# Optimization experiments

Measured on AMD Instinct MI355X. Metric: run time of the kernel, lower is better.

## Reference

```python
import jax, jax.numpy as jnp
import numpy as np

B, S, H = 2, 2048, 2048
NH, NKV, HD = 16, 8, 128
EPS = 1e-6
THETA = 10000.0
SCALE = HD ** -0.5


def setup_inputs() -> dict:
    key = jax.random.key(0)
    ks = jax.random.split(key, 6)
    return {
        "positions": jnp.tile(jnp.arange(S, dtype=jnp.int64 if jax.config.jax_enable_x64 else jnp.int32), (B, 1)),
        "hidden_states": jax.random.normal(ks[0], (B, S, H), jnp.float32),
        "residual": jax.random.normal(ks[1], (B, S, H), jnp.float32),
        "layernorm_weight": 1.0 + 0.02 * jax.random.normal(ks[2], (H,), jnp.float32),
        "qkv_weight": 0.02 * jax.random.normal(ks[3], ((NH + 2 * NKV) * HD, H), jnp.float32),
        "o_weight": 0.02 * jax.random.normal(ks[4], (H, NH * HD), jnp.float32),
        "q_norm_weight": 1.0 + 0.02 * jax.random.normal(ks[5], (HD,), jnp.float32),
        "k_norm_weight": jnp.ones((HD,), jnp.float32),
    }


def _rmsnorm(x, w, eps=EPS):
    return x * jax.lax.rsqrt(jnp.mean(x * x, axis=-1, keepdims=True) + eps) * w


def _rope(x, positions):
    # x: [B, S, h, HD]; neox-style rotate-half RoPE
    inv_freq = 1.0 / (THETA ** (jnp.arange(0, HD, 2, dtype=jnp.float32) / HD))
    ang = positions.astype(jnp.float32)[..., None] * inv_freq  # [B, S, HD/2]
    cos = jnp.cos(ang)[:, :, None, :]
    sin = jnp.sin(ang)[:, :, None, :]
    x1, x2 = jnp.split(x, 2, axis=-1)
    return jnp.concatenate([x1 * cos - x2 * sin, x2 * cos + x1 * sin], axis=-1)


def reference(positions, hidden_states, residual, layernorm_weight,
              qkv_weight, o_weight, q_norm_weight, k_norm_weight):
    # Fused RMSNorm + QKV projection (on unnormalized hidden_states)
    xn = _rmsnorm(hidden_states, layernorm_weight)
    qkv = jnp.einsum('bsh,oh->bso', xn, qkv_weight)  # [B, S, (NH+2*NKV)*HD]
    q, k, v = jnp.split(qkv, [NH * HD, (NH + NKV) * HD], axis=-1)
    q = q.reshape(B, S, NH, HD)
    k = k.reshape(B, S, NKV, HD)
    v = v.reshape(B, S, NKV, HD)
    # per-head q/k RMSNorm (q_norm in fused QKV kernel, k_norm inside attention)
    q = _rmsnorm(q, q_norm_weight)
    k = _rmsnorm(k, k_norm_weight)
    # RoPE
    q = _rope(q, positions)
    k = _rope(k, positions)
    # GQA: expand KV heads
    rep = NH // NKV
    k = jnp.repeat(k, rep, axis=2)
    v = jnp.repeat(v, rep, axis=2)
    # causal attention
    scores = jnp.einsum('bqhd,bkhd->bhqk', q, k) * SCALE
    causal = jnp.tril(jnp.ones((S, S), bool))
    scores = jnp.where(causal[None, None], scores, jnp.finfo(scores.dtype).min)
    probs = jax.nn.softmax(scores, axis=-1)
    attn = jnp.einsum('bhqk,bkhd->bqhd', probs, v).reshape(B, S, NH * HD)
    # fused output projection + residual add
    return jnp.einsum('bsd,hd->bsh', attn, o_weight) + residual
```

## Files before the change

kernel.cpp:

```cpp
#include <hip/hip_runtime.h>
#include <hip/hip_bf16.h>

typedef __attribute__((ext_vector_type(8))) short bf16x8;
typedef __attribute__((ext_vector_type(4))) float f32x4;

#define B_ 2
#define S_ 2048
#define H_ 2048
#define NH_ 16
#define NKV_ 8
#define HD_ 128
#define M_ (B_ * S_)
#define NQKV_ ((NH_ + 2 * NKV_) * HD_)
#define QK_SCALE 0.08838834764831845f

#define VMCNT(n) asm volatile("s_waitcnt vmcnt(" #n ")" ::: "memory")

__device__ __forceinline__ unsigned short f2bf(float f) {
  unsigned int u = __float_as_uint(f);
  u += 0x7fffu + ((u >> 16) & 1u);
  return (unsigned short)(u >> 16);
}
__device__ __forceinline__ float bf2f(unsigned short h) {
  return __uint_as_float(((unsigned int)h) << 16);
}
__device__ __forceinline__ unsigned int cvt_pk_bf16(float lo, float hi) {
  unsigned int r;
  asm("v_cvt_pk_bf16_f32 %0, %1, %2" : "=v"(r) : "v"(lo), "v"(hi));
  return r;
}
__device__ __forceinline__ void gload_lds16(const void* g, void* l) {
  __builtin_amdgcn_global_load_lds(
      (const __attribute__((address_space(1))) void*)g,
      (__attribute__((address_space(3))) void*)l, 16, 0, 0);
}

#define CONV_QKVW_F4 ((NQKV_ * H_) / 4)
#define CONV_TOT_F4 (CONV_QKVW_F4 + (H_ * NH_ * HD_) / 4)
#define ROPE_N (B_ * S_ * 64)
__global__ __launch_bounds__(256) void k_prep(
    const int* __restrict__ positions, const float* __restrict__ hidden,
    const float* __restrict__ ln_w, const float* __restrict__ qkv_w,
    const float* __restrict__ o_w, unsigned short* __restrict__ xn,
    unsigned short* __restrict__ qkvw_bf, unsigned short* __restrict__ owbf,
    float* __restrict__ cos_t, float* __restrict__ sin_t) {
  __shared__ float red[4];
  const int t = threadIdx.x;
  if (blockIdx.x < M_) {
    const int m = blockIdx.x;
    const float4* row = (const float4*)(hidden + (size_t)m * H_);
    float4 v0 = row[t];
    float4 v1 = row[t + 256];
    float ss = v0.x * v0.x + v0.y * v0.y + v0.z * v0.z + v0.w * v0.w +
               v1.x * v1.x + v1.y * v1.y + v1.z * v1.z + v1.w * v1.w;
#pragma unroll
    for (int mk = 1; mk < 64; mk <<= 1) ss += __shfl_xor(ss, mk);
    if ((t & 63) == 0) red[t >> 6] = ss;
    __syncthreads();
    ss = red[0] + red[1] + red[2] + red[3];
    const float sc = rsqrtf(ss * (1.0f / H_) + 1e-6f);
    const float4* wv = (const float4*)ln_w;
    float4 w0 = wv[t], w1 = wv[t + 256];
    ushort4 o0, o1;
    o0.x = f2bf(v0.x * sc * w0.x);
    o0.y = f2bf(v0.y * sc * w0.y);
    o0.z = f2bf(v0.z * sc * w0.z);
    o0.w = f2bf(v0.w * sc * w0.w);
    o1.x = f2bf(v1.x * sc * w1.x);
    o1.y = f2bf(v1.y * sc * w1.y);
    o1.z = f2bf(v1.z * sc * w1.z);
    o1.w = f2bf(v1.w * sc * w1.w);
    ushort4* orow = (ushort4*)(xn + (size_t)m * H_);
    orow[t] = o0;
    orow[t + 256] = o1;
  } else {
    const int L = (blockIdx.x - M_) * 256 + t;
    const int stride = 2048 * 256;
    for (int i = L; i < CONV_TOT_F4; i += stride) {
      const float4* src4;
      ushort4* dst4;
      int idx;
      if (i < CONV_QKVW_F4) {
        src4 = (const float4*)qkv_w;
        dst4 = (ushort4*)qkvw_bf;
        idx = i;
      } else {
        src4 = (const float4*)o_w;
        dst4 = (ushort4*)owbf;
        idx = i - CONV_QKVW_F4;
      }
      float4 v = src4[idx];
      ushort4 o;
      o.x = f2bf(v.x);
      o.y = f2bf(v.y);
      o.z = f2bf(v.z);
      o.w = f2bf(v.w);
      dst4[idx] = o;
    }
    if (L < ROPE_N) {
      const int d = L & 63;
      const int bs = L >> 6;
      float pos = (float)positions[bs];
      float inv_freq = powf(10000.0f, -(float)(2 * d) * (1.0f / HD_));
      float ang = pos * inv_freq;
      cos_t[L] = cosf(ang);
      sin_t[L] = sinf(ang);
    }
  }
}

template <int FMB>
__device__ __forceinline__ void load_a256(const unsigned short* sAb, int wm,
                                          int lr, int lg, bf16x8 (&af)[2][4]) {
#pragma unroll
  for (int kk = 0; kk < 2; ++kk) {
    const int pc = kk * 4 + lg;
#pragma unroll
    for (int i = 0; i < 4; ++i) {
      const int R = wm + (FMB + i) * 16 + lr;
      const int idx = ((R >> 6) & 1) * 8192 +
                      ((((R >> 7) << 6) | (R & 63)) << 6) +
                      ((pc ^ (R & 7)) << 3);
      af[kk][i] = *(const bf16x8*)&sAb[idx];
    }
  }
}
template <int FNB>
__device__ __forceinline__ void load_b256(const unsigned short* sBb, int wn,
                                          int lr, int lg, bf16x8 (&bfv)[2][2]) {
#pragma unroll
  for (int kk = 0; kk < 2; ++kk) {
    const int pc = kk * 4 + lg;
#pragma unroll
    for (int j = 0; j < 2; ++j) {
      const int R = wn + (FNB + j) * 16 + lr;
      const int idx = ((R >> 5) & 1) * 8192 +
                      ((((R >> 6) << 5) | (R & 31)) << 6) +
                      ((pc ^ (R & 7)) << 3);
      bfv[kk][j] = *(const bf16x8*)&sBb[idx];
    }
  }
}

template <int FMB, int FNB>
__device__ __forceinline__ void phase_mfma(const bf16x8 (&af)[2][4],
                                           const bf16x8 (&bfv)[2][2],
                                           f32x4 (&acc)[8][4]) {
#pragma unroll
  for (int kk = 0; kk < 2; ++kk)
#pragma unroll
    for (int i = 0; i < 4; ++i)
#pragma unroll
      for (int j = 0; j < 2; ++j)
        acc[FMB + i][FNB + j] = __builtin_amdgcn_mfma_f32_16x16x32_bf16(
            af[kk][i], bfv[kk][j], acc[FMB + i][FNB + j], 0, 0, 0);
}

__global__ __launch_bounds__(512, 2) void k_gemm256(
    const unsigned short* __restrict__ A, const unsigned short* __restrict__ Bt,
    unsigned short* __restrict__ C, int M, int N, int K) {
  __shared__ unsigned short sA[2][256 * 64];
  __shared__ unsigned short sB[2][256 * 64];
  const int tid = threadIdx.x;
  const int w = tid >> 6;
  const int l = tid & 63;
  const int lr = l & 15, lg = l >> 4;
  const int gx = gridDim.x;
  const int lin = blockIdx.y * gx + blockIdx.x;
  const int cpx = (gx * gridDim.y) >> 3;
  const int swz = (lin & 7) * cpx + (lin >> 3);
  const int m0 = (swz / gx) * 256, n0 = (swz % gx) * 256;
  const int wm = (w >> 2) * 128, wn = (w & 3) * 64;
  f32x4 acc[8][4] = {};

  auto stageA = [&](int t, int bufi, int h) {
    const int k0 = t * 64;
#pragma unroll
    for (int i = 0; i < 2; ++i) {
      const int L = i * 512 + tid;
      const int r = L >> 3;
      const int R = ((r >> 6) << 7) | (h << 6) | (r & 63);
      const int d = (L & 7) ^ (r & 7);
      gload_lds16(A + (size_t)(m0 + R) * K + k0 + d * 8,
                  (char*)sA[bufi] + h * 16384 +
                      (size_t)(i * 512 + w * 64) * 16);
    }
  };
  auto stageB = [&](int t, int bufi, int h) {
    const int k0 = t * 64;
#pragma unroll
    for (int i = 0; i < 2; ++i) {
      const int L = i * 512 + tid;
      const int r = L >> 3;
      const int R = ((r >> 5) << 6) | (h << 5) | (r & 31);
      const int d = (L & 7) ^ (r & 7);
      gload_lds16(Bt + (size_t)(n0 + R) * K + k0 + d * 8,
                  (char*)sB[bufi] + h * 16384 +
                      (size_t)(i * 512 + w * 64) * 16);
    }
  };

#define BARR()                          \
  __builtin_amdgcn_s_barrier();         \
  __builtin_amdgcn_sched_barrier(0)

  stageA(0, 0, 0);
  stageB(0, 0, 0);
  stageB(0, 0, 1);
  stageA(0, 0, 1);
  VMCNT(2);
  BARR();

  bf16x8 af[2][4];
  bf16x8 bfv0[2][2];
  bf16x8 bfv1[2][2];
  const int NT = K >> 6;
  for (int t = 0; t < NT; ++t) {
    const int bufi = t & 1;
    const int nb = bufi ^ 1;
    const bool st = (t + 1 < NT);
    load_a256<0>(sA[bufi], wm, lr, lg, af);
    load_b256<0>(sB[bufi], wn, lr, lg, bfv0);
    load_b256<2>(sB[bufi], wn, lr, lg, bfv1);
    if (st) {
      stageA(t + 1, nb, 0);
      stageB(t + 1, nb, 0);
    }
    __builtin_amdgcn_s_setprio(1);
    phase_mfma<0, 0>(af, bfv0, acc);
    phase_mfma<0, 2>(af, bfv1, acc);
    __builtin_amdgcn_s_setprio(0);
    if (st) {
      VMCNT(4);
    } else {
      VMCNT(0);
    }
    BARR();
    load_a256<4>(sA[bufi], wm, lr, lg, af);
    if (st) {
      stageB(t + 1, nb, 1);
      stageA(t + 1, nb, 1);
    }
    __builtin_amdgcn_s_setprio(1);
    phase_mfma<4, 2>(af, bfv1, acc);
    phase_mfma<4, 0>(af, bfv0, acc);
    __builtin_amdgcn_s_setprio(0);
    if (st) VMCNT(2);
    BARR();
  }

#pragma unroll
  for (int fm = 0; fm < 8; ++fm)
#pragma unroll
    for (int fn = 0; fn < 4; ++fn)
#pragma unroll
      for (int r = 0; r < 4; ++r) {
        const int row = m0 + wm + fm * 16 + lg * 4 + r;
        const int col = n0 + wn + fn * 16 + lr;
        C[(size_t)row * N + col] = f2bf(acc[fm][fn][r]);
      }
#undef BARR
}

template <int FMB>
__device__ __forceinline__ void load_ao(const unsigned short* sAb, int wm,
                                        int lr, int lg, bf16x8 (&af)[2][2]) {
#pragma unroll
  for (int kk = 0; kk < 2; ++kk) {
    const int pc = kk * 4 + lg;
#pragma unroll
    for (int i = 0; i < 2; ++i) {
      const int R = wm + (FMB + i) * 16 + lr;
      const int idx = ((R >> 5) & 1) * 8192 +
                      ((((R >> 6) << 5) | (R & 31)) << 6) +
                      ((pc ^ (R & 7)) << 3);
      af[kk][i] = *(const bf16x8*)&sAb[idx];
    }
  }
}
template <int FNB>
__device__ __forceinline__ void load_bo(const unsigned short* sBb, int wn,
                                        int lr, int lg, bf16x8 (&bfv)[2][2]) {
#pragma unroll
  for (int kk = 0; kk < 2; ++kk) {
    const int pc = kk * 4 + lg;
#pragma unroll
    for (int j = 0; j < 2; ++j) {
      const int R = wn + (FNB + j) * 16 + lr;
      const int idx = ((R >> 5) & 1) * 4096 +
                      ((((R >> 6) << 5) | (R & 31)) << 6) +
                      ((pc ^ (R & 7)) << 3);
      bfv[kk][j] = *(const bf16x8*)&sBb[idx];
    }
  }
}

template <int FMB, int FNB>
__device__ __forceinline__ void phase_mfma_o(const bf16x8 (&af)[2][2],
                                             const bf16x8 (&bfv)[2][2],
                                             f32x4 (&acc)[4][4]) {
#pragma unroll
  for (int kk = 0; kk < 2; ++kk)
#pragma unroll
    for (int i = 0; i < 2; ++i)
#pragma unroll
      for (int j = 0; j < 2; ++j)
        acc[FMB + i][FNB + j] = __builtin_amdgcn_mfma_f32_16x16x32_bf16(
            af[kk][i], bfv[kk][j], acc[FMB + i][FNB + j], 0, 0, 0);
}

__global__ __launch_bounds__(512, 1) void k_gemm_ores(
    const unsigned short* __restrict__ A, const unsigned short* __restrict__ Bt,
    float* __restrict__ Cout, const float* __restrict__ resid, int M, int N,
    int K) {
  __shared__ unsigned short sA[2][256 * 64];
  __shared__ unsigned short sB[2][128 * 64];
  const int tid = threadIdx.x;
  const int w = tid >> 6;
  const int l = tid & 63;
  const int lr = l & 15, lg = l >> 4;
  const int gx = gridDim.x;
  const int lin = blockIdx.y * gx + blockIdx.x;
  const int cpx = (gx * gridDim.y) >> 3;
  const int swz = (lin & 7) * cpx + (lin >> 3);
  const int m0 = (swz / gx) * 256, n0 = (swz % gx) * 128;
  const int wm = (w >> 1) * 64, wn = (w & 1) * 64;
  f32x4 acc[4][4] = {};

  auto stageAo = [&](int t, int bufi, int h) {
    const int k0 = t * 64;
#pragma unroll
    for (int i = 0; i < 2; ++i) {
      const int L = i * 512 + tid;
      const int r = L >> 3;
      const int R = ((r >> 5) << 6) | (h << 5) | (r & 31);
      const int d = (L & 7) ^ (r & 7);
      gload_lds16(A + (size_t)(m0 + R) * K + k0 + d * 8,
                  (char*)sA[bufi] + h * 16384 +
                      (size_t)(i * 512 + w * 64) * 16);
    }
  };
  auto stageBo = [&](int t, int bufi, int h) {
    const int k0 = t * 64;
    const int L = tid;
    const int r = L >> 3;
    const int R = ((r >> 5) << 6) | (h << 5) | (r & 31);
    const int d = (L & 7) ^ (r & 7);
    gload_lds16(Bt + (size_t)(n0 + R) * K + k0 + d * 8,
                (char*)sB[bufi] + h * 8192 + (size_t)(w * 64) * 16);
  };

#define BARR()                          \
  __builtin_amdgcn_s_barrier();         \
  __builtin_amdgcn_sched_barrier(0)

  stageAo(0, 0, 0);
  stageBo(0, 0, 0);
  stageBo(0, 0, 1);
  stageAo(0, 0, 1);
  VMCNT(2);
  BARR();

  bf16x8 af[2][2];
  bf16x8 bfv0[2][2];
  bf16x8 bfv1[2][2];
  const int NT = K >> 6;
  for (int t = 0; t < NT; ++t) {
    const int bufi = t & 1;
    const int nb = bufi ^ 1;
    const bool st = (t + 1 < NT);
    load_ao<0>(sA[bufi], wm, lr, lg, af);
    load_bo<0>(sB[bufi], wn, lr, lg, bfv0);
    load_bo<2>(sB[bufi], wn, lr, lg, bfv1);
    if (st) {
      stageAo(t + 1, nb, 0);
      stageBo(t + 1, nb, 0);
    }
    __builtin_amdgcn_s_setprio(1);
    phase_mfma_o<0, 0>(af, bfv0, acc);
    phase_mfma_o<0, 2>(af, bfv1, acc);
    __builtin_amdgcn_s_setprio(0);
    if (st) {
      VMCNT(3);
    } else {
      VMCNT(0);
    }
    BARR();
    load_ao<2>(sA[bufi], wm, lr, lg, af);
    if (st) {
      stageBo(t + 1, nb, 1);
      stageAo(t + 1, nb, 1);
    }
    __builtin_amdgcn_s_setprio(1);
    phase_mfma_o<2, 2>(af, bfv1, acc);
    phase_mfma_o<2, 0>(af, bfv0, acc);
    __builtin_amdgcn_s_setprio(0);
    if (st) VMCNT(2);
    BARR();
  }

#pragma unroll
  for (int i = 0; i < 4; ++i)
#pragma unroll
    for (int j = 0; j < 4; ++j)
#pragma unroll
      for (int r = 0; r < 4; ++r) {
        const int row = m0 + wm + i * 16 + lg * 4 + r;
        const int col = n0 + wn + j * 16 + lr;
        const size_t o = (size_t)row * N + col;
        Cout[o] = acc[i][j][r] + resid[o];
      }
#undef BARR
}

__global__ __launch_bounds__(256) void k_post(
    const unsigned short* __restrict__ qkv, const float* __restrict__ qw,
    const float* __restrict__ kw, const float* __restrict__ cos_t,
    const float* __restrict__ sin_t, unsigned short* __restrict__ qb,
    unsigned short* __restrict__ kb, unsigned short* __restrict__ vt_out) {
  __shared__ unsigned short tile[32][33];
  if (blockIdx.x < M_) {
    const int m = blockIdx.x;
    const int b = m >> 11, s = m & (S_ - 1);
    const int w = threadIdx.x >> 6, l = threadIdx.x & 63;
    const unsigned short* row = qkv + (size_t)m * NQKV_;
    const float c = cos_t[(size_t)m * 64 + l];
    const float sn = sin_t[(size_t)m * 64 + l];
    for (int hh = w * 6; hh < w * 6 + 6; ++hh) {
      int base, type;
      unsigned short* out;
      const float* nw;
      if (hh < NH_) {
        type = 0;
        base = hh * HD_;
        out = qb + ((size_t)(b * NH_ + hh) * S_ + s) * HD_;
        nw = qw;
      } else {
        int kh = hh - NH_;
        type = 1;
        base = NH_ * HD_ + kh * HD_;
        out = kb + ((size_t)(b * NKV_ + kh) * S_ + s) * HD_;
        nw = kw;
      }
      unsigned short r1 = row[base + l];
      unsigned short r2 = row[base + 64 + l];
      float x1 = bf2f(r1), x2 = bf2f(r2);
      float ss = x1 * x1 + x2 * x2;
#pragma unroll
      for (int mk = 1; mk < 64; mk <<= 1) ss += __shfl_xor(ss, mk);
      float sc = rsqrtf(ss * (1.0f / HD_) + 1e-6f);
      float y1 = x1 * sc * nw[l];
      float y2 = x2 * sc * nw[64 + l];
      float o1 = y1 * c - y2 * sn;
      float o2 = y2 * c + y1 * sn;
      if (type == 0) {
        o1 *= QK_SCALE;
        o2 *= QK_SCALE;
      }
      out[l] = f2bf(o1);
      out[64 + l] = f2bf(o2);
    }
  } else {
    const int n = blockIdx.x - M_;
    const int bx = n & 63, by = (n >> 6) & 3, bz = n >> 8;
    const int b = bz >> 3, kh = bz & 7;
    const unsigned short* src =
        qkv + (size_t)b * S_ * NQKV_ + (NH_ + NKV_ + kh) * HD_;
    unsigned short* dst = vt_out + (size_t)bz * S_ * HD_;
    const int tx = threadIdx.x & 31, ty = threadIdx.x >> 5;
#pragma unroll
    for (int i = ty; i < 32; i += 8)
      tile[i][tx] = src[(size_t)(bx * 32 + i) * NQKV_ + by * 32 + tx];
    __syncthreads();
#pragma unroll
    for (int i = ty; i < 32; i += 8)
      dst[(size_t)(by * 32 + i) * S_ + bx * 32 + tx] = tile[tx][i];
  }
}

#define MFIX 13.0f
__global__ __launch_bounds__(512, 4) void k_attn(
    const unsigned short* __restrict__ Q,
    const unsigned short* __restrict__ K,
    const unsigned short* __restrict__ VT,
    unsigned short* __restrict__ Oa) {
  __shared__ unsigned short kt[2][64 * 128];
  __shared__ unsigned short vt[2][128 * 64];
  __shared__ unsigned short pls[8 * 16 * 64];
  const int bh = blockIdx.y;
  const int b = bh >> 4, h = bh & 15;
  const int kvh = b * NKV_ + (h >> 1);
  const int xa = ((bh >> 4) & 1) ? (15 - blockIdx.x) : blockIdx.x;
  const int xb = 31 - xa;
  const int tid = threadIdx.x;
  const int w = tid >> 6, l = tid & 63;
  const int lr = l & 15, lg = l >> 4;
  const int wr = (w & 3) * 16;
  const int myx = (w < 4) ? xa : xb;
  const int q0m = myx * 64;

  bf16x8 qf[4];
  {
    const unsigned short* Qp = Q + ((size_t)bh * S_ + q0m + wr) * HD_;
#pragma unroll
    for (int tt = 0; tt < 4; ++tt)
      qf[tt] = *(const bf16x8*)(Qp + (size_t)lr * HD_ + tt * 32 + lg * 8);
  }
  f32x4 ao[8] = {};
  float lsum = 0.f;
  const unsigned short* Kp = K + (size_t)kvh * S_ * HD_;
  const unsigned short* Vp = VT + (size_t)kvh * HD_ * S_;
  unsigned short* pw = pls + w * 1024;
  const int psw = (lr & 7) << 1;

  auto stage = [&](int t, int bufi) {
    const int k0 = t * 64;
#pragma unroll
    for (int i = 0; i < 2; ++i) {
      const int chunk = i * 512 + tid;
      {
        const int r = chunk >> 4, p = chunk & 15;
        const int d = p ^ (r & 7);
        gload_lds16(Kp + (size_t)(k0 + r) * HD_ + d * 8,
                    (char*)kt[bufi] + (size_t)(i * 512 + w * 64) * 16);
      }
      {
        const int r = chunk >> 3, p = chunk & 7;
        const int d = p ^ (r & 7);
        gload_lds16(Vp + (size_t)r * S_ + k0 + d * 8,
                    (char*)vt[bufi] + (size_t)(i * 512 + w * 64) * 16);
      }
    }
  };

  auto process = [&](int t, int bufi, bool diag) {
    const unsigned short* ktb = kt[bufi];
    const unsigned short* vtb = vt[bufi];
    f32x4 sc[4] = {};
    __builtin_amdgcn_s_setprio(1);
#pragma unroll
    for (int j = 0; j < 4; ++j)
#pragma unroll
      for (int tt = 0; tt < 4; ++tt) {
        bf16x8 kf = *(const bf16x8*)&ktb[(j * 16 + lr) * 128 +
                                         (((tt * 4 + lg) ^ (lr & 7)) << 3)];
        sc[j] =
            __builtin_amdgcn_mfma_f32_16x16x32_bf16(kf, qf[tt], sc[j], 0, 0, 0);
      }
    __builtin_amdgcn_s_setprio(0);
    if (diag) {
      const int qg = q0m + wr + lr;
      const int kvb = t * 64 + lg * 4;
#pragma unroll
      for (int j = 0; j < 4; ++j)
#pragma unroll
        for (int r = 0; r < 4; ++r)
          if (kvb + j * 16 + r > qg) sc[j][r] = -1e30f;
    }
#pragma unroll
    for (int j = 0; j < 4; ++j) {
      float p0 = __expf(sc[j][0] - MFIX);
      float p1 = __expf(sc[j][1] - MFIX);
      float p2 = __expf(sc[j][2] - MFIX);
      float p3 = __expf(sc[j][3] - MFIX);
      lsum += (p0 + p1) + (p2 + p3);
      uint2 v;
      v.x = cvt_pk_bf16(p0, p1);
      v.y = cvt_pk_bf16(p2, p3);
      const int g = (4 * j + lg) ^ psw;
      *(uint2*)&pw[lr * 64 + g * 4] = v;
    }
    __builtin_amdgcn_s_setprio(1);
#pragma unroll
    for (int ks = 0; ks < 2; ++ks) {
      const int g0 = (8 * ks + 2 * lg) ^ psw;
      bf16x8 pf = *(const bf16x8*)&pw[lr * 64 + g0 * 4];
#pragma unroll
      for (int dj = 0; dj < 8; ++dj) {
        bf16x8 vf = *(const bf16x8*)&vtb[(dj * 16 + lr) * 64 +
                                         (((ks * 4 + lg) ^ (lr & 7)) << 3)];
        ao[dj] =
            __builtin_amdgcn_mfma_f32_16x16x32_bf16(vf, pf, ao[dj], 0, 0, 0);
      }
    }
    __builtin_amdgcn_s_setprio(0);
  };

  stage(0, 0);
  __syncthreads();
  int cur = 0;
  for (int t = 0; t <= xb; ++t) {
    if (t < xb) stage(t + 1, cur ^ 1);
    if (t <= myx) process(t, cur, t == myx);
    __syncthreads();
    cur ^= 1;
  }

  lsum += __shfl_xor(lsum, 16);
  lsum += __shfl_xor(lsum, 32);
  const float inv = 1.0f / lsum;
  const int sg = q0m + wr + lr;
  unsigned short* orow = Oa + ((size_t)b * S_ + sg) * (NH_ * HD_) + h * HD_;
#pragma unroll
  for (int dj = 0; dj < 8; ++dj) {
    ushort4 ov;
    ov.x = f2bf(ao[dj][0] * inv);
    ov.y = f2bf(ao[dj][1] * inv);
    ov.z = f2bf(ao[dj][2] * inv);
    ov.w = f2bf(ao[dj][3] * inv);
    *(ushort4*)&orow[dj * 16 + lg * 4] = ov;
  }
}

extern "C" void kernel_launch(void* const* d_in, const int* in_sizes, int n_in,
                              void* d_out, int out_size, void* d_ws,
                              size_t ws_size, hipStream_t stream) {
  const int* positions = (const int*)d_in[0];
  const float* hidden = (const float*)d_in[1];
  const float* residual = (const float*)d_in[2];
  const float* ln_w = (const float*)d_in[3];
  const float* qkv_w = (const float*)d_in[4];
  const float* o_w = (const float*)d_in[5];
  const float* q_nw = (const float*)d_in[6];
  const float* k_nw = (const float*)d_in[7];

  char* ws = (char*)d_ws;
  const size_t SZ_XN = (size_t)M_ * H_ * 2;
  const size_t SZ_QKVW = (size_t)NQKV_ * H_ * 2;
  const size_t SZ_OW = (size_t)H_ * (NH_ * HD_) * 2;
  const size_t SZ_QKV = (size_t)M_ * NQKV_ * 2;
  const size_t SZ_KB = (size_t)B_ * NKV_ * S_ * HD_ * 2;
  const size_t SZ_COS = (size_t)B_ * S_ * 64 * 4;

  unsigned short* xn = (unsigned short*)(ws);
  unsigned short* q_buf = (unsigned short*)(ws);
  unsigned short* qkvw_bf = (unsigned short*)(ws + SZ_XN);
  unsigned short* k_buf = (unsigned short*)(ws + SZ_XN);
  unsigned short* owbf = (unsigned short*)(ws + SZ_XN + SZ_QKVW);
  unsigned short* qkv_bf = (unsigned short*)(ws + SZ_XN + SZ_QKVW + SZ_OW);
  unsigned short* attn_o = qkv_bf;
  unsigned short* vt_buf =
      (unsigned short*)(ws + SZ_XN + SZ_QKVW + SZ_OW + SZ_QKV);
  float* cos_t = (float*)(ws + SZ_XN + SZ_QKVW + SZ_OW + SZ_QKV + SZ_KB);
  float* sin_t = (float*)((char*)cos_t + SZ_COS);

  k_prep<<<M_ + 2048, 256, 0, stream>>>(positions, hidden, ln_w, qkv_w, o_w,
                                        xn, qkvw_bf, owbf, cos_t, sin_t);
  k_gemm256<<<dim3(NQKV_ / 256, M_ / 256), 512, 0, stream>>>(
      xn, qkvw_bf, qkv_bf, M_, NQKV_, H_);
  k_post<<<M_ + 4096, 256, 0, stream>>>(qkv_bf, q_nw, k_nw, cos_t, sin_t,
                                        q_buf, k_buf, vt_buf);
  k_attn<<<dim3(16, B_ * NH_), 512, 0, stream>>>(q_buf, k_buf, vt_buf, attn_o);
  k_gemm_ores<<<dim3((NH_ * HD_) / 128, M_ / 256), 512, 0, stream>>>(
      attn_o, owbf, (float*)d_out, residual, M_, NH_ * HD_, H_);
}
```

Before: 204.6 us.

## Split attention into per-tile blocks and overlap o_weight conversion with attention

The attention kernel goes from 512-thread blocks that paired two query tiles for causal load balance to 256-thread blocks, one per 64-row query tile. The KV tile shrinks to 32 keys and the LDS buffers and swizzles are resized to match. Blocks are launched heaviest-first so long tiles start early. The fp32-to-bf16 conversion of o_weight moves out of the prep kernel into an extra column of attention blocks, shortening prep and overlapping the conversion with attention. The cost is more loop iterations with less work per barrier, and the grid is more imbalanced across blocks.

```diff
diff --git a/kernel.cpp b/kernel.cpp
--- a/kernel.cpp
+++ b/kernel.cpp
@@ -36,13 +36,11 @@
 }
 
 #define CONV_QKVW_F4 ((NQKV_ * H_) / 4)
-#define CONV_TOT_F4 (CONV_QKVW_F4 + (H_ * NH_ * HD_) / 4)
 #define ROPE_N (B_ * S_ * 64)
 __global__ __launch_bounds__(256) void k_prep(
     const int* __restrict__ positions, const float* __restrict__ hidden,
     const float* __restrict__ ln_w, const float* __restrict__ qkv_w,
-    const float* __restrict__ o_w, unsigned short* __restrict__ xn,
-    unsigned short* __restrict__ qkvw_bf, unsigned short* __restrict__ owbf,
+    unsigned short* __restrict__ xn, unsigned short* __restrict__ qkvw_bf,
     float* __restrict__ cos_t, float* __restrict__ sin_t) {
   __shared__ float red[4];
   const int t = threadIdx.x;
@@ -76,26 +74,14 @@
   } else {
     const int L = (blockIdx.x - M_) * 256 + t;
     const int stride = 2048 * 256;
-    for (int i = L; i < CONV_TOT_F4; i += stride) {
-      const float4* src4;
-      ushort4* dst4;
-      int idx;
-      if (i < CONV_QKVW_F4) {
-        src4 = (const float4*)qkv_w;
-        dst4 = (ushort4*)qkvw_bf;
-        idx = i;
-      } else {
-        src4 = (const float4*)o_w;
-        dst4 = (ushort4*)owbf;
-        idx = i - CONV_QKVW_F4;
-      }
-      float4 v = src4[idx];
+    for (int i = L; i < CONV_QKVW_F4; i += stride) {
+      float4 v = ((const float4*)qkv_w)[i];
       ushort4 o;
       o.x = f2bf(v.x);
       o.y = f2bf(v.y);
       o.z = f2bf(v.z);
       o.w = f2bf(v.w);
-      dst4[idx] = o;
+      ((ushort4*)qkvw_bf)[i] = o;
     }
     if (L < ROPE_N) {
       const int d = L & 63;
@@ -479,29 +465,43 @@
 }
 
 #define MFIX 13.0f
-__global__ __launch_bounds__(512, 4) void k_attn(
+__global__ __launch_bounds__(256, 4) void k_attn(
     const unsigned short* __restrict__ Q,
     const unsigned short* __restrict__ K,
     const unsigned short* __restrict__ VT,
-    unsigned short* __restrict__ Oa) {
-  __shared__ unsigned short kt[2][64 * 128];
-  __shared__ unsigned short vt[2][128 * 64];
-  __shared__ unsigned short pls[8 * 16 * 64];
+    unsigned short* __restrict__ Oa,
+    const float* __restrict__ o_w, unsigned short* __restrict__ owbf) {
+  if (blockIdx.x == 32) {
+    const int L = blockIdx.y * 256 + threadIdx.x;
+    const int stride = 32 * 256;
+    const int n4 = (H_ * NH_ * HD_) / 4;
+    for (int i = L; i < n4; i += stride) {
+      float4 v = ((const float4*)o_w)[i];
+      ushort4 o;
+      o.x = f2bf(v.x);
+      o.y = f2bf(v.y);
+      o.z = f2bf(v.z);
+      o.w = f2bf(v.w);
+      ((ushort4*)owbf)[i] = o;
+    }
+    return;
+  }
+  __shared__ unsigned short kt[2][32 * 128];
+  __shared__ unsigned short vt[2][128 * 32];
+  __shared__ unsigned short pls[4 * 16 * 32];
   const int bh = blockIdx.y;
   const int b = bh >> 4, h = bh & 15;
   const int kvh = b * NKV_ + (h >> 1);
-  const int xa = ((bh >> 4) & 1) ? (15 - blockIdx.x) : blockIdx.x;
-  const int xb = 31 - xa;
+  const int xq = 31 - blockIdx.x;
+  const int q0 = xq * 64;
   const int tid = threadIdx.x;
   const int w = tid >> 6, l = tid & 63;
   const int lr = l & 15, lg = l >> 4;
-  const int wr = (w & 3) * 16;
-  const int myx = (w < 4) ? xa : xb;
-  const int q0m = myx * 64;
+  const int qrow = q0 + w * 16;
 
   bf16x8 qf[4];
   {
-    const unsigned short* Qp = Q + ((size_t)bh * S_ + q0m + wr) * HD_;
+    const unsigned short* Qp = Q + ((size_t)bh * S_ + qrow) * HD_;
 #pragma unroll
     for (int tt = 0; tt < 4; ++tt)
       qf[tt] = *(const bf16x8*)(Qp + (size_t)lr * HD_ + tt * 32 + lg * 8);
@@ -510,36 +510,36 @@
   float lsum = 0.f;
   const unsigned short* Kp = K + (size_t)kvh * S_ * HD_;
   const unsigned short* Vp = VT + (size_t)kvh * HD_ * S_;
-  unsigned short* pw = pls + w * 1024;
-  const int psw = (lr & 7) << 1;
+  unsigned short* pw = pls + w * 512;
+  const int sw = (lr & 3) << 1;
 
   auto stage = [&](int t, int bufi) {
-    const int k0 = t * 64;
+    const int k0 = t * 32;
 #pragma unroll
     for (int i = 0; i < 2; ++i) {
-      const int chunk = i * 512 + tid;
-      {
-        const int r = chunk >> 4, p = chunk & 15;
-        const int d = p ^ (r & 7);
-        gload_lds16(Kp + (size_t)(k0 + r) * HD_ + d * 8,
-                    (char*)kt[bufi] + (size_t)(i * 512 + w * 64) * 16);
-      }
-      {
-        const int r = chunk >> 3, p = chunk & 7;
-        const int d = p ^ (r & 7);
-        gload_lds16(Vp + (size_t)r * S_ + k0 + d * 8,
-                    (char*)vt[bufi] + (size_t)(i * 512 + w * 64) * 16);
-      }
+      const int c = i * 256 + tid;
+      const int r = c >> 4, p = c & 15;
+      const int dd = p ^ (r & 7);
+      gload_lds16(Kp + (size_t)(k0 + r) * HD_ + dd * 8,
+                  (char*)kt[bufi] + (size_t)(i * 256 + w * 64) * 16);
+    }
+#pragma unroll
+    for (int i = 0; i < 2; ++i) {
+      const int c = i * 256 + tid;
+      const int r = c >> 2, p = c & 3;
+      const int dd = p ^ ((r >> 1) & 3);
+      gload_lds16(Vp + (size_t)r * S_ + k0 + dd * 8,
+                  (char*)vt[bufi] + (size_t)(i * 256 + w * 64) * 16);
     }
   };
 
   auto process = [&](int t, int bufi, bool diag) {
     const unsigned short* ktb = kt[bufi];
     const unsigned short* vtb = vt[bufi];
-    f32x4 sc[4] = {};
+    f32x4 sc[2] = {};
     __builtin_amdgcn_s_setprio(1);
 #pragma unroll
-    for (int j = 0; j < 4; ++j)
+    for (int j = 0; j < 2; ++j)
 #pragma unroll
       for (int tt = 0; tt < 4; ++tt) {
         bf16x8 kf = *(const bf16x8*)&ktb[(j * 16 + lr) * 128 +
@@ -549,16 +549,16 @@
       }
     __builtin_amdgcn_s_setprio(0);
     if (diag) {
-      const int qg = q0m + wr + lr;
-      const int kvb = t * 64 + lg * 4;
-#pragma unroll
-      for (int j = 0; j < 4; ++j)
+      const int qg = qrow + lr;
+      const int kvb = t * 32 + lg * 4;
+#pragma unroll
+      for (int j = 0; j < 2; ++j)
 #pragma unroll
         for (int r = 0; r < 4; ++r)
           if (kvb + j * 16 + r > qg) sc[j][r] = -1e30f;
     }
 #pragma unroll
-    for (int j = 0; j < 4; ++j) {
+    for (int j = 0; j < 2; ++j) {
       float p0 = __expf(sc[j][0] - MFIX);
       float p1 = __expf(sc[j][1] - MFIX);
       float p2 = __expf(sc[j][2] - MFIX);
@@ -567,18 +567,17 @@
       uint2 v;
       v.x = cvt_pk_bf16(p0, p1);
       v.y = cvt_pk_bf16(p2, p3);
-      const int g = (4 * j + lg) ^ psw;
-      *(uint2*)&pw[lr * 64 + g * 4] = v;
+      const int g = (j * 4 + lg) ^ sw;
+      *(uint2*)&pw[lr * 32 + g * 4] = v;
     }
     __builtin_amdgcn_s_setprio(1);
-#pragma unroll
-    for (int ks = 0; ks < 2; ++ks) {
-      const int g0 = (8 * ks + 2 * lg) ^ psw;
-      bf16x8 pf = *(const bf16x8*)&pw[lr * 64 + g0 * 4];
+    {
+      const int g0 = (2 * lg) ^ sw;
+      bf16x8 pf = *(const bf16x8*)&pw[lr * 32 + g0 * 4];
 #pragma unroll
       for (int dj = 0; dj < 8; ++dj) {
-        bf16x8 vf = *(const bf16x8*)&vtb[(dj * 16 + lr) * 64 +
-                                         (((ks * 4 + lg) ^ (lr & 7)) << 3)];
+        bf16x8 vf = *(const bf16x8*)&vtb[(dj * 16 + lr) * 32 +
+                                         ((lg ^ ((lr >> 1) & 3)) << 3)];
         ao[dj] =
             __builtin_amdgcn_mfma_f32_16x16x32_bf16(vf, pf, ao[dj], 0, 0, 0);
       }
@@ -586,12 +585,14 @@
     __builtin_amdgcn_s_setprio(0);
   };
 
+  const int NTT = 2 * (xq + 1);
+  const int tlim = (qrow + 15) >> 5;
   stage(0, 0);
   __syncthreads();
   int cur = 0;
-  for (int t = 0; t <= xb; ++t) {
-    if (t < xb) stage(t + 1, cur ^ 1);
-    if (t <= myx) process(t, cur, t == myx);
+  for (int t = 0; t < NTT; ++t) {
+    if (t + 1 < NTT) stage(t + 1, cur ^ 1);
+    if (t <= tlim) process(t, cur, (t * 32 + 31) > qrow);
     __syncthreads();
     cur ^= 1;
   }
@@ -599,7 +600,7 @@
   lsum += __shfl_xor(lsum, 16);
   lsum += __shfl_xor(lsum, 32);
   const float inv = 1.0f / lsum;
-  const int sg = q0m + wr + lr;
+  const int sg = qrow + lr;
   unsigned short* orow = Oa + ((size_t)b * S_ + sg) * (NH_ * HD_) + h * HD_;
 #pragma unroll
   for (int dj = 0; dj < 8; ++dj) {
@@ -644,13 +645,14 @@
   float* cos_t = (float*)(ws + SZ_XN + SZ_QKVW + SZ_OW + SZ_QKV + SZ_KB);
   float* sin_t = (float*)((char*)cos_t + SZ_COS);
 
-  k_prep<<<M_ + 2048, 256, 0, stream>>>(positions, hidden, ln_w, qkv_w, o_w,
-                                        xn, qkvw_bf, owbf, cos_t, sin_t);
+  k_prep<<<M_ + 2048, 256, 0, stream>>>(positions, hidden, ln_w, qkv_w, xn,
+                                        qkvw_bf, cos_t, sin_t);
   k_gemm256<<<dim3(NQKV_ / 256, M_ / 256), 512, 0, stream>>>(
       xn, qkvw_bf, qkv_bf, M_, NQKV_, H_);
   k_post<<<M_ + 4096, 256, 0, stream>>>(qkv_bf, q_nw, k_nw, cos_t, sin_t,
                                         q_buf, k_buf, vt_buf);
-  k_attn<<<dim3(16, B_ * NH_), 512, 0, stream>>>(q_buf, k_buf, vt_buf, attn_o);
+  k_attn<<<dim3(33, B_ * NH_), 256, 0, stream>>>(q_buf, k_buf, vt_buf, attn_o,
+                                                 o_w, owbf);
   k_gemm_ores<<<dim3((NH_ * HD_) / 128, M_ / 256), 512, 0, stream>>>(
       attn_o, owbf, (float*)d_out, residual, M_, NH_ * HD_, H_);
 }
```

Measured after the change: 217.3 us. 6.2% more time.
